# Optimization experiments

Hardware: AMD Instinct MI355X
Metric: run time of the kernel (lower is better)

## Reference

```python
import jax, jax.numpy as jnp
import numpy as np

MARGIN = 0.5


def setup_inputs() -> dict:
    key = jax.random.key(0)
    k1, k2, k3 = jax.random.split(key, 3)
    B, D = 8192, 128
    anchor = jax.random.normal(k1, (B, D), dtype=jnp.float32)
    positive = jax.random.normal(k2, (B, D), dtype=jnp.float32)
    labels = jax.random.randint(k3, (B,), 0, 100, dtype=jnp.int64)
    return {"anchor": anchor, "positive": positive, "labels": labels}


def _l2_normalize(x, eps=1e-12):
    # matches F.normalize(p=2, dim=1): x / max(||x||, eps)
    n = jnp.sqrt(jnp.sum(x * x, axis=1, keepdims=True))
    return x / jnp.maximum(n, eps)


def reference(anchor, positive, labels):
    a = _l2_normalize(anchor)   # [B, D]
    p = _l2_normalize(positive)  # [B, D]

    # pairwise euclidean distances among normalized anchors:
    # ||a_i - a_j||^2 = 2 - 2 a_i . a_j  (unit vectors)
    gram = jnp.einsum('id,jd->ij', a, a)              # [B, B]
    dist = jnp.sqrt(jnp.maximum(2.0 - 2.0 * gram, 0.0))

    # mask out same-label pairs (includes diagonal)
    same = labels[None, :] == labels[:, None]
    dist = jnp.where(same, jnp.inf, dist)

    min_dist = jnp.min(dist, axis=1)                  # [B]
    neg_dist = min_dist * min_dist                    # squared distance to hard negative

    pos_dist = jnp.sum((a - p) ** 2, axis=1)          # [B]

    loss = jax.nn.relu(pos_dist - neg_dist + MARGIN)
    return jnp.mean(loss)
```

## Files before the change

kernel.cpp:

```cpp
#include <hip/hip_runtime.h>
#include <stdint.h>

#define NROWS 8192
#define DIM 128
#define NTILE 1056

typedef __bf16 bf16x8 __attribute__((ext_vector_type(8)));
typedef float floatx4 __attribute__((ext_vector_type(4)));

static __device__ __forceinline__ unsigned short f2bf(float f) {
    unsigned int u = __float_as_uint(f);
    unsigned int r = (u + 0x7FFFu + ((u >> 16) & 1u)) >> 16;
    return (unsigned short)r;
}

static __device__ __forceinline__ int swz(int g) {
    return (g & ~15) | ((g & 15) ^ ((g >> 4) & 7));
}

static __device__ __forceinline__ void gload_lds16(const uint4* g, uint4* l) {
    __builtin_amdgcn_global_load_lds(
        (const __attribute__((address_space(1))) void*)g,
        (__attribute__((address_space(3))) void*)l, 16, 0, 0);
}

static __device__ __forceinline__ int cumtile(int rb) {
    return 32 * rb - (rb * rb - 2 * rb + (rb & 1)) / 4;
}

__global__ __launch_bounds__(256) void normalize_kernel(
    const float* __restrict__ anchor, const float* __restrict__ positive,
    unsigned short* __restrict__ a_hat, float* __restrict__ pos_ws,
    float* __restrict__ out)
{
    if (blockIdx.x == 0 && threadIdx.x == 0) *out = 0.0f;

    const int wave = threadIdx.x >> 6;
    const int lane = threadIdx.x & 63;
    const int row  = blockIdx.x * 4 + wave;

    const float2* arow = (const float2*)(anchor   + row * DIM);
    const float2* prow = (const float2*)(positive + row * DIM);
    float2 a = arow[lane];
    float2 p = prow[lane];

    float sa  = a.x * a.x + a.y * a.y;
    float sp  = p.x * p.x + p.y * p.y;
    float sap = a.x * p.x + a.y * p.y;
    #pragma unroll
    for (int off = 32; off; off >>= 1) {
        sa  += __shfl_xor(sa,  off);
        sp  += __shfl_xor(sp,  off);
        sap += __shfl_xor(sap, off);
    }
    float na  = fmaxf(sqrtf(sa), 1e-12f);
    float npn = fmaxf(sqrtf(sp), 1e-12f);
    float inv = 1.0f / na;

    ushort2 pack;
    pack.x = f2bf(a.x * inv);
    pack.y = f2bf(a.y * inv);
    ((ushort2*)a_hat)[row * 64 + lane] = pack;

    if (lane == 0)
        pos_ws[row] = 2.0f - 2.0f * sap / (na * npn);
}

__global__ __launch_bounds__(256) void gram_kernel(
    const unsigned short* __restrict__ a_hat, const int* __restrict__ labels,
    float* __restrict__ P, float* __restrict__ Q)
{
    const int tid  = threadIdx.x;
    const int lane = tid & 63;
    const int wave = tid >> 6;
    const int quad = lane >> 4;
    const int l15  = lane & 15;

    const int bid = blockIdx.x;
    int rb = (int)(64.0f - 2.0f * sqrtf(1024.0f - (float)bid));
    rb = rb < 0 ? 0 : (rb > 63 ? 63 : rb);
    while (cumtile(rb) > bid) --rb;
    while (cumtile(rb + 1) <= bid) ++rb;
    const int cc = (rb >> 1) + (bid - cumtile(rb));

    const int rowBase = rb * 128 + wave * 32;
    const int colBase = cc * 256;

    const uint4* A = (const uint4*)a_hat;
    const uint4* Gsrc = A + colBase * 16;

    __shared__ uint4  smem[4096];
    __shared__ float  wcol[4][256];

    #pragma unroll
    for (int i = 0; i < 16; ++i) {
        const int s = i * 256 + wave * 64 + lane;
        gload_lds16(Gsrc + swz(s), &smem[i * 256 + wave * 64]);
    }

    bf16x8 afrag[2][4];
    #pragma unroll
    for (int ms = 0; ms < 2; ++ms) {
        const int r = rowBase + ms * 16 + l15;
        #pragma unroll
        for (int k = 0; k < 4; ++k)
            afrag[ms][k] = __builtin_bit_cast(bf16x8, A[r * 16 + k * 4 + quad]);
    }

    int4 rlab[2];
    #pragma unroll
    for (int ms = 0; ms < 2; ++ms)
        rlab[ms] = *(const int4*)(labels + rowBase + ms * 16 + quad * 4);

    float gmax[2][4];
    #pragma unroll
    for (int ms = 0; ms < 2; ++ms)
        #pragma unroll
        for (int e = 0; e < 4; ++e)
            gmax[ms][e] = -4.0f;

    __syncthreads();

    #pragma unroll
    for (int cb = 0; cb < 8; ++cb) {
        const int C = colBase + cb * 32;
        const int clab0 = labels[C + l15];
        const int clab1 = labels[C + 16 + l15];

        bf16x8 bfrag[2][4];
        #pragma unroll
        for (int ns = 0; ns < 2; ++ns) {
            const int c = ns * 16 + l15;
            #pragma unroll
            for (int k = 0; k < 4; ++k) {
                const int g = cb * 512 + c * 16 + k * 4 + quad;
                bfrag[ns][k] = __builtin_bit_cast(bf16x8, smem[swz(g)]);
            }
        }

        #pragma unroll
        for (int ns = 0; ns < 2; ++ns) {
            const int cl = ns ? clab1 : clab0;
            float cmax = -4.0f;
            #pragma unroll
            for (int ms = 0; ms < 2; ++ms) {
                floatx4 acc = {0.f, 0.f, 0.f, 0.f};
                #pragma unroll
                for (int k = 0; k < 4; ++k)
                    acc = __builtin_amdgcn_mfma_f32_16x16x32_bf16(
                              afrag[ms][k], bfrag[ns][k], acc, 0, 0, 0);
                #pragma unroll
                for (int e = 0; e < 4; ++e) {
                    const int rle = (e == 0) ? rlab[ms].x : (e == 1) ? rlab[ms].y
                                  : (e == 2) ? rlab[ms].z : rlab[ms].w;
                    float v = (cl != rle) ? acc[e] : -4.0f;
                    gmax[ms][e] = fmaxf(gmax[ms][e], v);
                    cmax        = fmaxf(cmax, v);
                }
            }
            cmax = fmaxf(cmax, __shfl_xor(cmax, 16));
            cmax = fmaxf(cmax, __shfl_xor(cmax, 32));
            if (quad == 0)
                wcol[wave][cb * 32 + ns * 16 + l15] = cmax;
        }
    }

    #pragma unroll
    for (int ms = 0; ms < 2; ++ms) {
        #pragma unroll
        for (int e = 0; e < 4; ++e) {
            float v = gmax[ms][e];
            #pragma unroll
            for (int off = 1; off < 16; off <<= 1)
                v = fmaxf(v, __shfl_xor(v, off));
            if (l15 == 0)
                P[cc * NROWS + rowBase + ms * 16 + quad * 4 + e] = v;
        }
    }

    __syncthreads();
    {
        float m = fmaxf(fmaxf(wcol[0][tid], wcol[1][tid]),
                        fmaxf(wcol[2][tid], wcol[3][tid]));
        Q[rb * NROWS + colBase + tid] = m;
    }
}

__global__ __launch_bounds__(256) void loss_kernel(
    const float* __restrict__ pos_ws, const float* __restrict__ P,
    const float* __restrict__ Q, float* __restrict__ out)
{
    const int tid  = threadIdx.x;
    const int lane = tid & 63;
    const int wave = tid >> 6;
    const int j    = tid & 15;
    const int g16  = tid >> 4;
    const int row  = blockIdx.x * 16 + g16;
    const int r256 = row >> 8;

    float g = -4.0f;
    for (int c = r256 + j; c < 32; c += 16)
        g = fmaxf(g, P[c * NROWS + row]);
    const int rmax = (2 * r256 + 1 < 63) ? 2 * r256 + 1 : 63;
    for (int t = j; t <= rmax; t += 16)
        g = fmaxf(g, Q[t * NROWS + row]);

    #pragma unroll
    for (int off = 1; off < 16; off <<= 1)
        g = fmaxf(g, __shfl_xor(g, off));

    float part = 0.0f;
    if (j == 0) {
        float neg = fmaxf(2.0f - 2.0f * g, 0.0f);
        part = fmaxf(pos_ws[row] - neg + 0.5f, 0.0f);
    }
    part += __shfl_xor(part, 16);
    part += __shfl_xor(part, 32);

    __shared__ float wsum[4];
    if (lane == 0) wsum[wave] = part;
    __syncthreads();
    if (tid == 0)
        atomicAdd(out, (wsum[0] + wsum[1] + wsum[2] + wsum[3]) * (1.0f / 8192.0f));
}

extern "C" void kernel_launch(void* const* d_in, const int* in_sizes, int n_in,
                              void* d_out, int out_size, void* d_ws, size_t ws_size,
                              hipStream_t stream) {
    const float* anchor   = (const float*)d_in[0];
    const float* positive = (const float*)d_in[1];
    const int*   labels   = (const int*)d_in[2];
    float* out = (float*)d_out;

    char* ws = (char*)d_ws;
    unsigned short* a_hat  = (unsigned short*)ws;
    float*          pos_ws = (float*)(ws + 2 * 1024 * 1024);
    float*          P      = (float*)(ws + 4 * 1024 * 1024);
    float*          Q      = (float*)(ws + 5 * 1024 * 1024);

    normalize_kernel<<<NROWS / 4, 256, 0, stream>>>(anchor, positive, a_hat, pos_ws, out);
    gram_kernel<<<NTILE, 256, 0, stream>>>(a_hat, labels, P, Q);
    loss_kernel<<<NROWS / 16, 256, 0, stream>>>(pos_ws, P, Q, out);
}
```

Before: 102.6 us.

## Double-buffer column tiles via registers instead of bulk global-to-LDS preload

Replaces the upfront 64KB global_load_lds preload of the column tile with a two-slot LDS buffer of 8KB that is filled through registers one 32-column chunk ahead of the compute. This shrinks LDS use per block and adds a launch-bounds occupancy hint, so more blocks can be resident, and loads overlap the MFMA work. In exchange it adds a barrier on every chunk, register staging and the loss of the unrolled loop. The cumtile formula is also rewritten without division.

```diff
diff --git a/kernel.cpp b/kernel.cpp
--- a/kernel.cpp
+++ b/kernel.cpp
@@ -18,14 +18,9 @@
     return (g & ~15) | ((g & 15) ^ ((g >> 4) & 7));
 }
 
-static __device__ __forceinline__ void gload_lds16(const uint4* g, uint4* l) {
-    __builtin_amdgcn_global_load_lds(
-        (const __attribute__((address_space(1))) void*)g,
-        (__attribute__((address_space(3))) void*)l, 16, 0, 0);
-}
-
 static __device__ __forceinline__ int cumtile(int rb) {
-    return 32 * rb - (rb * rb - 2 * rb + (rb & 1)) / 4;
+    const int q = rb >> 1;
+    return 32 * rb - q * q + ((rb & 1) ? 0 : q);
 }
 
 __global__ __launch_bounds__(256) void normalize_kernel(
@@ -66,7 +61,7 @@
         pos_ws[row] = 2.0f - 2.0f * sap / (na * npn);
 }
 
-__global__ __launch_bounds__(256) void gram_kernel(
+__global__ __launch_bounds__(256, 4) void gram_kernel(
     const unsigned short* __restrict__ a_hat, const int* __restrict__ labels,
     float* __restrict__ P, float* __restrict__ Q)
 {
@@ -77,26 +72,23 @@
     const int l15  = lane & 15;
 
     const int bid = blockIdx.x;
-    int rb = (int)(64.0f - 2.0f * sqrtf(1024.0f - (float)bid));
+    int rb = (int)(64.0f - 2.0f * sqrtf(fmaxf(1024.0f - (float)bid, 0.0f)));
     rb = rb < 0 ? 0 : (rb > 63 ? 63 : rb);
     while (cumtile(rb) > bid) --rb;
     while (cumtile(rb + 1) <= bid) ++rb;
-    const int cc = (rb >> 1) + (bid - cumtile(rb));
+    const int c = (rb >> 1) + (bid - cumtile(rb));
 
     const int rowBase = rb * 128 + wave * 32;
-    const int colBase = cc * 256;
-
-    const uint4* A = (const uint4*)a_hat;
-    const uint4* Gsrc = A + colBase * 16;
-
-    __shared__ uint4  smem[4096];
+    const int colBase = c * 256;
+
+    const uint4* A  = (const uint4*)a_hat;
+    const uint4* Gp = A + colBase * 16;
+
+    __shared__ uint4  smem[2][512];
     __shared__ float  wcol[4][256];
 
-    #pragma unroll
-    for (int i = 0; i < 16; ++i) {
-        const int s = i * 256 + wave * 64 + lane;
-        gload_lds16(Gsrc + swz(s), &smem[i * 256 + wave * 64]);
-    }
+    uint4 p0 = Gp[tid];
+    uint4 p1 = Gp[tid + 256];
 
     bf16x8 afrag[2][4];
     #pragma unroll
@@ -112,6 +104,10 @@
     for (int ms = 0; ms < 2; ++ms)
         rlab[ms] = *(const int4*)(labels + rowBase + ms * 16 + quad * 4);
 
+    smem[0][swz(tid)]       = p0;
+    smem[0][swz(tid + 256)] = p1;
+    __syncthreads();
+
     float gmax[2][4];
     #pragma unroll
     for (int ms = 0; ms < 2; ++ms)
@@ -119,10 +115,14 @@
         for (int e = 0; e < 4; ++e)
             gmax[ms][e] = -4.0f;
 
-    __syncthreads();
-
-    #pragma unroll
     for (int cb = 0; cb < 8; ++cb) {
+        const int cur = cb & 1;
+
+        if (cb < 7) {
+            p0 = Gp[(cb + 1) * 512 + tid];
+            p1 = Gp[(cb + 1) * 512 + tid + 256];
+        }
+
         const int C = colBase + cb * 32;
         const int clab0 = labels[C + l15];
         const int clab1 = labels[C + 16 + l15];
@@ -130,12 +130,11 @@
         bf16x8 bfrag[2][4];
         #pragma unroll
         for (int ns = 0; ns < 2; ++ns) {
-            const int c = ns * 16 + l15;
+            const int cl = ns * 16 + l15;
             #pragma unroll
-            for (int k = 0; k < 4; ++k) {
-                const int g = cb * 512 + c * 16 + k * 4 + quad;
-                bfrag[ns][k] = __builtin_bit_cast(bf16x8, smem[swz(g)]);
-            }
+            for (int k = 0; k < 4; ++k)
+                bfrag[ns][k] = __builtin_bit_cast(bf16x8,
+                                   smem[cur][swz(cl * 16 + k * 4 + quad)]);
         }
 
         #pragma unroll
@@ -163,6 +162,12 @@
             if (quad == 0)
                 wcol[wave][cb * 32 + ns * 16 + l15] = cmax;
         }
+
+        if (cb < 7) {
+            smem[cur ^ 1][swz(tid)]       = p0;
+            smem[cur ^ 1][swz(tid + 256)] = p1;
+            __syncthreads();
+        }
     }
 
     #pragma unroll
@@ -174,7 +179,7 @@
             for (int off = 1; off < 16; off <<= 1)
                 v = fmaxf(v, __shfl_xor(v, off));
             if (l15 == 0)
-                P[cc * NROWS + rowBase + ms * 16 + quad * 4 + e] = v;
+                P[c * NROWS + rowBase + ms * 16 + quad * 4 + e] = v;
         }
     }
 
```

After: 109.7 us. 6.9% more time.
